# Performance work log

Hardware: AMD Instinct MI355X
Metric: run time of the kernel (lower is better)

## Reference

```python
import jax, jax.numpy as jnp
import numpy as np
from jax import lax

NUM_IN = 128
NUM_HIDDEN = 1024
NUM_OUT = 128
BATCH = 64
SEQ_LEN = 512


def setup_inputs() -> dict:
    key = jax.random.key(0)
    ks = jax.random.split(key, 10)
    s_ih = 1.0 / np.sqrt(NUM_IN)
    s_hh = 1.0 / np.sqrt(NUM_HIDDEN)
    init_state_C = np.sqrt(3.0 / (2.0 * NUM_HIDDEN))
    return {
        "x": jax.random.normal(ks[0], (BATCH, SEQ_LEN, NUM_IN), jnp.float32),
        "h0": jax.random.normal(ks[1], (BATCH, NUM_HIDDEN), jnp.float32) * init_state_C,
        # RNNCell params (torch layout: [hidden, in], [hidden, hidden])
        "W_ih": jax.random.uniform(ks[2], (NUM_HIDDEN, NUM_IN), jnp.float32, -s_hh, s_hh),
        "b_ih": jax.random.uniform(ks[3], (NUM_HIDDEN,), jnp.float32, -s_hh, s_hh),
        "W_hh": jax.random.uniform(ks[4], (NUM_HIDDEN, NUM_HIDDEN), jnp.float32, -s_hh, s_hh),
        "b_hh": jax.random.uniform(ks[5], (NUM_HIDDEN,), jnp.float32, -s_hh, s_hh),
        # SequenceModel head: Linear(H,H)+ReLU then Linear(H,num_out)
        "W1": jax.random.uniform(ks[6], (NUM_HIDDEN, NUM_HIDDEN), jnp.float32, -s_hh, s_hh),
        "b1": jax.random.uniform(ks[7], (NUM_HIDDEN,), jnp.float32, -s_hh, s_hh),
        "W2": jax.random.uniform(ks[8], (NUM_OUT, NUM_HIDDEN), jnp.float32, -s_hh, s_hh),
        "b2": jax.random.uniform(ks[9], (NUM_OUT,), jnp.float32, -s_hh, s_hh),
    }


def reference(x, h0, W_ih, b_ih, W_hh, b_hh, W1, b1, W2, b2):
    # RNNCell: h_t = tanh(x_t @ W_ih^T + b_ih + h_{t-1} @ W_hh^T + b_hh)
    xs = jnp.swapaxes(x, 0, 1)  # [S, B, num_in]

    def step(h, x_t):
        h_new = jnp.tanh(x_t @ W_ih.T + b_ih + h @ W_hh.T + b_hh)
        return h_new, None

    h_last, _ = lax.scan(step, h0, xs)
    # single_output head: MLP(Linear+ReLU) then fc
    mlp = jax.nn.relu(h_last @ W1.T + b1)
    outputs_o = mlp @ W2.T + b2  # [B, num_out]
    return outputs_o, h_last
```

## Files before the change

### kernel.cpp

```cpp
#include <hip/hip_runtime.h>

#define HID   1024
#define NIN   128
#define BSZ   64
#define SLEN  512
#define KTOT  1152
#define NBLK  64
#define NGRID 256
#define NOUT  128

typedef short          bf16x8 __attribute__((ext_vector_type(8)));
typedef unsigned short us8    __attribute__((ext_vector_type(8)));
typedef float          f32x4  __attribute__((ext_vector_type(4)));
typedef unsigned int   u32x2  __attribute__((ext_vector_type(2)));

__device__ __forceinline__ unsigned short rne_bf16(float f) {
    unsigned int u = __builtin_bit_cast(unsigned int, f);
    u += 0x7FFFu + ((u >> 16) & 1u);
    return (unsigned short)(u >> 16);
}
__device__ __forceinline__ float bf2f(unsigned short h) {
    unsigned int u = ((unsigned int)h) << 16;
    return __builtin_bit_cast(float, u);
}

#define OFF_WLO 1179648
#define OFF_H0  2359296
#define OFF_H1  2424832
#define OFF_F32 2490368
#define OFF_SIG 2752512
#define SIG_N   (SLEN * 64 + 64)

__global__ void __launch_bounds__(256) prep(
    const float* __restrict__ W_ih, const float* __restrict__ W_hh,
    const float* __restrict__ h0, unsigned short* __restrict__ wsu)
{
    const int g = blockIdx.x * 256 + threadIdx.x;
    if (g < SIG_N) ((unsigned*)(wsu + OFF_SIG))[g] = 0u;
    if (g < 1024 * KTOT) {
        const int j = g / KTOT;
        const int k = g - j * KTOT;
        const float v = (k < HID) ? W_hh[j * HID + k] : W_ih[j * NIN + (k - HID)];
        const unsigned short hi = rne_bf16(v);
        wsu[g] = hi;
        wsu[OFF_WLO + g] = rne_bf16(v - bf2f(hi));
    } else if (g < 1024 * KTOT + 65536) {
        const int e = g - 1024 * KTOT;
        wsu[OFF_H0 + e] = rne_bf16(h0[e]);
    }
}

#define LDH(dst, IMM) \
    asm volatile("global_load_dwordx4 %0, %1, off offset:" #IMM " sc0 sc1" \
                 : "=v"(dst) : "v"(hb))
__device__ __forceinline__ void st16f_llc(float* p, f32x4 v) {
    asm volatile("global_store_dwordx4 %0, %1, off sc0 sc1" :: "v"(p), "v"(v) : "memory");
}

__global__ void __launch_bounds__(512, 2) rnn_mfma(
    const float* __restrict__ x,
    const float* __restrict__ b_ih, const float* __restrict__ b_hh,
    const float* __restrict__ W1,   const float* __restrict__ b1,
    const float* __restrict__ W2,   const float* __restrict__ b2,
    float* __restrict__ out, unsigned short* __restrict__ wsu)
{
    const int tid  = threadIdx.x, bid = blockIdx.x;
    const int lane = tid & 63, wave = tid >> 6;
    unsigned* sig = (unsigned*)(wsu + OFF_SIG);

    __shared__ float red[4][32][36];
    __shared__ char  lds_pad[65536];
    ((volatile char*)lds_pad)[tid & 1023] = 0;

    if (bid >= NBLK) {
        const unsigned* fl = sig + (size_t)(SLEN - 1) * 64;
        float a = 1.0f + (float)tid * 1e-7f, c = 0.9999f;
        const float b = 1.000001f;
        for (int it = 0; it < (1 << 22); ++it) {
            #pragma unroll
            for (int u = 0; u < 64; ++u) {
                a = __builtin_fmaf(a, b, 1e-9f);
                c = __builtin_fmaf(c, b, -1e-9f);
            }
            if ((it & 7) == 0) {
                unsigned f = 0;
                if (lane == 0)
                    asm volatile("global_load_dword %0, %1, off sc0 sc1\n\ts_waitcnt vmcnt(0)"
                                 : "=v"(f) : "v"(fl) : "memory");
                if (__shfl(f, 0)) break;
            }
        }
        asm volatile("" :: "v"(a), "v"(c));
        return;
    }

    const int lr = lane & 15, lg = lane >> 4;
    const int kc = wave & 3, mh = wave >> 2;
    const int jb = bid >> 1, bh = bid & 1;
    const int j0 = jb * 32;

    const unsigned short* __restrict__ Whi = wsu;
    const unsigned short* __restrict__ Wlo = wsu + OFF_WLO;
    unsigned short* hA = wsu + OFF_H0;
    unsigned short* hB = wsu + OFF_H1;
    float* hfp = (float*)(wsu + OFF_F32);
    float* mlp = hfp + 65536;

    bf16x8 wh0[9], wl0[9], wh1[9], wl1[9];
    #pragma unroll
    for (int ks = 0; ks < 9; ++ks) {
        const int col = (ks < 8) ? (kc * 256 + ks * 32 + lg * 8)
                                 : (1024 + kc * 32 + lg * 8);
        wh0[ks] = *(const bf16x8*)(Whi + (size_t)(j0 + lr) * KTOT + col);
        wl0[ks] = *(const bf16x8*)(Wlo + (size_t)(j0 + lr) * KTOT + col);
        wh1[ks] = *(const bf16x8*)(Whi + (size_t)(j0 + 16 + lr) * KTOT + col);
        wl1[ks] = *(const bf16x8*)(Wlo + (size_t)(j0 + 16 + lr) * KTOT + col);
    }

    const int rb  = tid >> 3;
    const int rj0 = (tid & 7) * 4;
    const int rjg = j0 + rj0;
    f32x4 bias4;
    #pragma unroll
    for (int i = 0; i < 4; ++i)
        bias4[i] = b_ih[rjg + i] + b_hh[rjg + i];

    const int brow = bh * 32 + mh * 16 + lr;

    for (int t = 1; t <= SLEN; ++t) {
        const unsigned short* cur = ((t - 1) & 1) ? hB : hA;
        unsigned short* nxt = (t & 1) ? hB : hA;

        const float* xp = x + ((size_t)brow * SLEN + (t - 1)) * NIN + kc * 32 + lg * 8;
        const f32x4 x0 = *(const f32x4*)xp;
        const f32x4 x1 = *(const f32x4*)(xp + 4);
        bf16x8 xh, xl;
        #pragma unroll
        for (int e = 0; e < 4; ++e) {
            const unsigned short a = rne_bf16(x0[e]);
            xh[e] = (short)a; xl[e] = (short)rne_bf16(x0[e] - bf2f(a));
            const unsigned short b = rne_bf16(x1[e]);
            xh[4 + e] = (short)b; xl[4 + e] = (short)rne_bf16(x1[e] - bf2f(b));
        }
        const f32x4 z = {0.f, 0.f, 0.f, 0.f};
        f32x4 acc0, acc1;
        acc0 = __builtin_amdgcn_mfma_f32_16x16x32_bf16(xh, wh0[8], z, 0, 0, 0);
        acc0 = __builtin_amdgcn_mfma_f32_16x16x32_bf16(xh, wl0[8], acc0, 0, 0, 0);
        acc0 = __builtin_amdgcn_mfma_f32_16x16x32_bf16(xl, wh0[8], acc0, 0, 0, 0);
        acc1 = __builtin_amdgcn_mfma_f32_16x16x32_bf16(xh, wh1[8], z, 0, 0, 0);
        acc1 = __builtin_amdgcn_mfma_f32_16x16x32_bf16(xh, wl1[8], acc1, 0, 0, 0);
        acc1 = __builtin_amdgcn_mfma_f32_16x16x32_bf16(xl, wh1[8], acc1, 0, 0, 0);

        if (t > 1) {
            const unsigned* base = sig + (size_t)(t - 2) * 64 + kc * 16 + bh;
            unsigned f = 1;
            if (lane < 8) f = __hip_atomic_load(base + 2 * lane, __ATOMIC_RELAXED,
                                                __HIP_MEMORY_SCOPE_AGENT);
            int it = 0;
            while (!__all(f != 0)) {
                __builtin_amdgcn_s_sleep(2);
                f = 1;
                if (lane < 8) f = __hip_atomic_load(base + 2 * lane, __ATOMIC_RELAXED,
                                                    __HIP_MEMORY_SCOPE_AGENT);
                if (++it > (1 << 17)) break;
            }
        }

        const unsigned short* hb = cur + brow * 1024 + kc * 256 + lg * 8;
        bf16x8 h0v, h1v, h2v, h3v, h4v, h5v, h6v, h7v;
        LDH(h0v,   0); LDH(h1v,  64);
        LDH(h2v, 128); LDH(h3v, 192);
        LDH(h4v, 256); LDH(h5v, 320);
        LDH(h6v, 384); LDH(h7v, 448);
        asm volatile("s_waitcnt vmcnt(0)" ::: "memory");
        __builtin_amdgcn_sched_barrier(0);

        #define GRAN(g, hv)                                                          \
            acc0 = __builtin_amdgcn_mfma_f32_16x16x32_bf16(hv, wh0[g], acc0, 0,0,0); \
            acc0 = __builtin_amdgcn_mfma_f32_16x16x32_bf16(hv, wl0[g], acc0, 0,0,0); \
            acc1 = __builtin_amdgcn_mfma_f32_16x16x32_bf16(hv, wh1[g], acc1, 0,0,0); \
            acc1 = __builtin_amdgcn_mfma_f32_16x16x32_bf16(hv, wl1[g], acc1, 0,0,0);
        GRAN(0, h0v) GRAN(1, h1v) GRAN(2, h2v) GRAN(3, h3v)
        GRAN(4, h4v) GRAN(5, h5v) GRAN(6, h6v) GRAN(7, h7v)
        #undef GRAN

        #pragma unroll
        for (int r = 0; r < 4; ++r) {
            red[kc][mh * 16 + lg * 4 + r][lr]      = acc0[r];
            red[kc][mh * 16 + lg * 4 + r][16 + lr] = acc1[r];
        }
        __syncthreads();
        if (tid < 256) {
            const f32x4 r0 = *(const f32x4*)&red[0][rb][rj0];
            const f32x4 r1 = *(const f32x4*)&red[1][rb][rj0];
            const f32x4 r2 = *(const f32x4*)&red[2][rb][rj0];
            const f32x4 r3 = *(const f32x4*)&red[3][rb][rj0];
            float v[4];
            #pragma unroll
            for (int i = 0; i < 4; ++i)
                v[i] = tanhf(r0[i] + r1[i] + r2[i] + r3[i] + bias4[i]);
            const int bg = bh * 32 + rb;
            unsigned short* hp = nxt + bg * 1024 + rjg;
            const u32x2 hw = { (unsigned)rne_bf16(v[0]) | ((unsigned)rne_bf16(v[1]) << 16),
                               (unsigned)rne_bf16(v[2]) | ((unsigned)rne_bf16(v[3]) << 16) };
            asm volatile("global_store_dwordx2 %0, %1, off sc0 sc1"
                         :: "v"(hp), "v"(hw) : "memory");
            if (t == SLEN) {
                const f32x4 vv = {v[0], v[1], v[2], v[3]};
                st16f_llc(hfp + (size_t)bg * HID + rjg, vv);
                st16f_llc(out + BSZ * NOUT + (size_t)bg * HID + rjg, vv);
            }
        }
        __syncthreads();
        if (tid == 0) {
            if (t == SLEN)
                __hip_atomic_store(sig + (size_t)(t - 1) * 64 + bid, 1u,
                                   __ATOMIC_RELEASE, __HIP_MEMORY_SCOPE_AGENT);
            else
                __hip_atomic_store(sig + (size_t)(t - 1) * 64 + bid, 1u,
                                   __ATOMIC_RELAXED, __HIP_MEMORY_SCOPE_AGENT);
        }
    }

    if (wave == 0) {
        const unsigned* s = sig + (size_t)(SLEN - 1) * 64;
        unsigned f = (lane < NBLK) ? 0u : 1u;
        int it = 0;
        while (!__all(f != 0)) {
            __builtin_amdgcn_s_sleep(2);
            f = 1;
            if (lane < NBLK) f = __hip_atomic_load(s + lane, __ATOMIC_RELAXED,
                                                   __HIP_MEMORY_SCOPE_AGENT);
            if (++it > (1 << 18)) break;
        }
        __builtin_amdgcn_fence(__ATOMIC_ACQUIRE, "agent");
    }
    __syncthreads();

    {
        const int jl = tid & 31, bq = tid >> 5;
        const int jg = j0 + jl;
        const f32x4* w1r = (const f32x4*)(W1 + (size_t)jg * HID);
        const int bA = bh * 32 + bq, bB = bA + 16;
        const f32x4* hA4 = (const f32x4*)(hfp + (size_t)bA * HID);
        const f32x4* hB4 = (const f32x4*)(hfp + (size_t)bB * HID);
        float a0 = 0.f, a1 = 0.f;
        for (int k4 = 0; k4 < HID / 4; ++k4) {
            const f32x4 wv = w1r[k4];
            const f32x4 u = hA4[k4], w = hB4[k4];
            a0 += wv[0]*u[0] + wv[1]*u[1] + wv[2]*u[2] + wv[3]*u[3];
            a1 += wv[0]*w[0] + wv[1]*w[1] + wv[2]*w[2] + wv[3]*w[3];
        }
        const float bj = b1[jg];
        mlp[(size_t)bA * HID + jg] = fmaxf(a0 + bj, 0.f);
        mlp[(size_t)bB * HID + jg] = fmaxf(a1 + bj, 0.f);
    }
    __syncthreads();
    if (tid == 0)
        __hip_atomic_store(sig + (size_t)SLEN * 64 + bid, 1u,
                           __ATOMIC_RELEASE, __HIP_MEMORY_SCOPE_AGENT);

    if (bid < 16) {
        if (wave == 0) {
            const unsigned* s = sig + (size_t)SLEN * 64;
            unsigned f = (lane < NBLK) ? 0u : 1u;
            int it = 0;
            while (!__all(f != 0)) {
                __builtin_amdgcn_s_sleep(2);
                f = 1;
                if (lane < NBLK) f = __hip_atomic_load(s + lane, __ATOMIC_RELAXED,
                                                       __HIP_MEMORY_SCOPE_AGENT);
                if (++it > (1 << 18)) break;
            }
            __builtin_amdgcn_fence(__ATOMIC_ACQUIRE, "agent");
        }
        __syncthreads();
        const int g = bid * 512 + tid;
        const int b = g >> 7, o = g & 127;
        const f32x4* w2r = (const f32x4*)(W2 + (size_t)o * HID);
        const f32x4* mr  = (const f32x4*)(mlp + (size_t)b * HID);
        float a = 0.f;
        for (int k4 = 0; k4 < HID / 4; ++k4) {
            const f32x4 wv = w2r[k4], mv = mr[k4];
            a += wv[0]*mv[0] + wv[1]*mv[1] + wv[2]*mv[2] + wv[3]*mv[3];
        }
        out[b * NOUT + o] = a + b2[o];
    }
}

extern "C" void kernel_launch(void* const* d_in, const int* in_sizes, int n_in,
                              void* d_out, int out_size, void* d_ws, size_t ws_size,
                              hipStream_t stream) {
    const float* x    = (const float*)d_in[0];
    const float* h0   = (const float*)d_in[1];
    const float* W_ih = (const float*)d_in[2];
    const float* b_ih = (const float*)d_in[3];
    const float* W_hh = (const float*)d_in[4];
    const float* b_hh = (const float*)d_in[5];
    const float* W1   = (const float*)d_in[6];
    const float* b1   = (const float*)d_in[7];
    const float* W2   = (const float*)d_in[8];
    const float* b2   = (const float*)d_in[9];
    float* out = (float*)d_out;
    unsigned short* wsu = (unsigned short*)d_ws;

    const int nprep = 1024 * KTOT + 65536;
    prep<<<(nprep + 255) / 256, 256, 0, stream>>>(W_ih, W_hh, h0, wsu);

    void* args[] = {&x, &b_ih, &b_hh, &W1, &b1, &W2, &b2, &out, &wsu};
    hipLaunchCooperativeKernel(reinterpret_cast<void*>(rnn_mfma),
                               dim3(NGRID), dim3(512), args, 0, stream);
}
```

Baseline: 2.090 ms.

## Switch to per-wave step flags so consumers wait only on needed producers

Each of the four writer waves now publishes its own relaxed flag per step, after waiting for its own stores. This removes the block-wide barrier and the single-thread flag store at the end of every step. Consumers poll 16 finer-grained flags covering just the rows they read, with a shorter sleep between polls. The flag array grows fourfold and a barrier is added before the LDS reduction writes to protect reuse of the shared buffer. Correctness now rests on a relaxed store after s_waitcnt being enough for cross-block visibility, and the final step no longer uses a release store.

```diff
diff --git a/kernel.cpp b/kernel.cpp
--- a/kernel.cpp
+++ b/kernel.cpp
@@ -29,7 +29,8 @@
 #define OFF_H1  2424832
 #define OFF_F32 2490368
 #define OFF_SIG 2752512
-#define SIG_N   (SLEN * 64 + 64)
+#define SIG_MLP 131072
+#define SIG_N   131136
 
 __global__ void __launch_bounds__(256) prep(
     const float* __restrict__ W_ih, const float* __restrict__ W_hh,
@@ -73,7 +74,7 @@
     ((volatile char*)lds_pad)[tid & 1023] = 0;
 
     if (bid >= NBLK) {
-        const unsigned* fl = sig + (size_t)(SLEN - 1) * 64;
+        const unsigned* fl = sig + (size_t)(SLEN - 1) * 256;
         float a = 1.0f + (float)tid * 1e-7f, c = 0.9999f;
         const float b = 1.000001f;
         for (int it = 0; it < (1 << 22); ++it) {
@@ -152,16 +153,17 @@
         acc1 = __builtin_amdgcn_mfma_f32_16x16x32_bf16(xl, wh1[8], acc1, 0, 0, 0);
 
         if (t > 1) {
-            const unsigned* base = sig + (size_t)(t - 2) * 64 + kc * 16 + bh;
+            const unsigned* base = sig + (((size_t)(t - 2) * 2 + bh) * 4) * 32;
+            const int fofs = (2 * mh + (lane >> 3)) * 32 + kc * 8 + (lane & 7);
             unsigned f = 1;
-            if (lane < 8) f = __hip_atomic_load(base + 2 * lane, __ATOMIC_RELAXED,
-                                                __HIP_MEMORY_SCOPE_AGENT);
+            if (lane < 16) f = __hip_atomic_load(base + fofs, __ATOMIC_RELAXED,
+                                                 __HIP_MEMORY_SCOPE_AGENT);
             int it = 0;
             while (!__all(f != 0)) {
-                __builtin_amdgcn_s_sleep(2);
+                __builtin_amdgcn_s_sleep(1);
                 f = 1;
-                if (lane < 8) f = __hip_atomic_load(base + 2 * lane, __ATOMIC_RELAXED,
-                                                    __HIP_MEMORY_SCOPE_AGENT);
+                if (lane < 16) f = __hip_atomic_load(base + fofs, __ATOMIC_RELAXED,
+                                                     __HIP_MEMORY_SCOPE_AGENT);
                 if (++it > (1 << 17)) break;
             }
         }
@@ -184,12 +186,14 @@
         GRAN(4, h4v) GRAN(5, h5v) GRAN(6, h6v) GRAN(7, h7v)
         #undef GRAN
 
+        __syncthreads();
         #pragma unroll
         for (int r = 0; r < 4; ++r) {
             red[kc][mh * 16 + lg * 4 + r][lr]      = acc0[r];
             red[kc][mh * 16 + lg * 4 + r][16 + lr] = acc1[r];
         }
         __syncthreads();
+
         if (tid < 256) {
             const f32x4 r0 = *(const f32x4*)&red[0][rb][rj0];
             const f32x4 r1 = *(const f32x4*)&red[1][rb][rj0];
@@ -210,28 +214,28 @@
                 st16f_llc(hfp + (size_t)bg * HID + rjg, vv);
                 st16f_llc(out + BSZ * NOUT + (size_t)bg * HID + rjg, vv);
             }
-        }
-        __syncthreads();
-        if (tid == 0) {
-            if (t == SLEN)
-                __hip_atomic_store(sig + (size_t)(t - 1) * 64 + bid, 1u,
-                                   __ATOMIC_RELEASE, __HIP_MEMORY_SCOPE_AGENT);
-            else
-                __hip_atomic_store(sig + (size_t)(t - 1) * 64 + bid, 1u,
-                                   __ATOMIC_RELAXED, __HIP_MEMORY_SCOPE_AGENT);
+            asm volatile("s_waitcnt vmcnt(0)" ::: "memory");
+            if (lane == 0) {
+                unsigned* fp = sig + (((size_t)(t - 1) * 2 + bh) * 4 + wave) * 32 + jb;
+                __hip_atomic_store(fp, 1u, __ATOMIC_RELAXED, __HIP_MEMORY_SCOPE_AGENT);
+            }
         }
     }
 
     if (wave == 0) {
-        const unsigned* s = sig + (size_t)(SLEN - 1) * 64;
-        unsigned f = (lane < NBLK) ? 0u : 1u;
+        const unsigned* s = sig + (size_t)(SLEN - 1) * 256;
+        unsigned ok = 0;
         int it = 0;
-        while (!__all(f != 0)) {
-            __builtin_amdgcn_s_sleep(2);
-            f = 1;
-            if (lane < NBLK) f = __hip_atomic_load(s + lane, __ATOMIC_RELAXED,
-                                                   __HIP_MEMORY_SCOPE_AGENT);
+        while (!__all(ok)) {
+            ok = 1;
+            #pragma unroll
+            for (int q = 0; q < 4; ++q) {
+                const unsigned f = __hip_atomic_load(s + lane * 4 + q, __ATOMIC_RELAXED,
+                                                     __HIP_MEMORY_SCOPE_AGENT);
+                ok &= (f != 0) ? 1u : 0u;
+            }
             if (++it > (1 << 18)) break;
+            if (!__all(ok)) __builtin_amdgcn_s_sleep(2);
         }
         __builtin_amdgcn_fence(__ATOMIC_ACQUIRE, "agent");
     }
@@ -257,12 +261,12 @@
     }
     __syncthreads();
     if (tid == 0)
-        __hip_atomic_store(sig + (size_t)SLEN * 64 + bid, 1u,
+        __hip_atomic_store(sig + SIG_MLP + bid, 1u,
                            __ATOMIC_RELEASE, __HIP_MEMORY_SCOPE_AGENT);
 
     if (bid < 16) {
         if (wave == 0) {
-            const unsigned* s = sig + (size_t)SLEN * 64;
+            const unsigned* s = sig + SIG_MLP;
             unsigned f = (lane < NBLK) ? 0u : 1u;
             int it = 0;
             while (!__all(f != 0)) {
```

After: 2.586 ms. 23.7% more time.
